# Optimization experiments

Measured on AMD Instinct MI355X. Metric: run time of the kernel, lower is better.

Reference implementation:

```python
import jax, jax.numpy as jnp
import numpy as np

B, D, CL, QL = 32, 128, 1024, 512


def setup_inputs() -> dict:
    key = jax.random.key(0)
    kC, kQ, kW = jax.random.split(key, 3)
    C = jax.random.normal(kC, (B, D, CL), dtype=jnp.float32)
    Q = jax.random.normal(kQ, (B, D, QL), dtype=jnp.float32)
    # xavier_normal_ on (B*CL, 1, 3D): std = sqrt(2 / (fan_in + fan_out)) = sqrt(2/(1+3D))
    std = (2.0 / (1.0 + 3.0 * D)) ** 0.5
    W = jax.random.normal(kW, (B * CL, 1, 3 * D), dtype=jnp.float32) * std
    return {"C": C, "Q": Q, "W": W}


def reference(C, Q, W):
    # C: (B, D, CL), Q: (B, D, QL), W: (B*CL, 1, 3D)
    b, d, cl = C.shape
    Ct = jnp.transpose(C, (0, 2, 1))   # (B, CL, D)
    Qt = jnp.transpose(Q, (0, 2, 1))   # (B, QL, D)
    Wr = W.reshape(b, cl, 3 * d)
    wq, wc, wqc = Wr[..., :d], Wr[..., d:2 * d], Wr[..., 2 * d:]
    # Trilinear similarity: S[b,c,q] = wq[b,c].Q[b,q] + wc[b,c].C[b,c] + wqc[b,c].(C[b,c]*Q[b,q])
    S = (jnp.einsum('bcd,bqd->bcq', wq, Qt)
         + jnp.sum(wc * Ct, axis=-1, keepdims=True)
         + jnp.einsum('bcd,bqd->bcq', wqc * Ct, Qt))   # (B, CL, QL)
    S1 = jax.nn.softmax(S, axis=2)  # over queries
    S2 = jax.nn.softmax(S, axis=1)  # over context
    A = jnp.einsum('bcq,bqd->bcd', S1, Qt)             # (B, CL, D)
    # B = (S1 @ S2^T) @ C, reassociated as S1 @ (S2^T @ C) to avoid (CL,CL) intermediate
    S2tC = jnp.einsum('bkq,bkd->bqd', S2, Ct)          # (B, QL, D)
    Bm = jnp.einsum('bcq,bqd->bcd', S1, S2tC)          # (B, CL, D)
    out = jnp.concatenate([Ct, A, Ct * A, Ct * Bm], axis=2)  # (B, CL, 4D)
    # dropout is identity in eval mode
    return jnp.transpose(out, (0, 2, 1))               # (B, 4D, CL)
```

## Files before the change

### kernel.cpp

```cpp
#include <hip/hip_runtime.h>
#include <hip/hip_bf16.h>
#include <cstddef>

#define B_  32
#define D_  128
#define CL_ 1024
#define QL_ 512

using short8  = __attribute__((ext_vector_type(8))) short;
using short4v = __attribute__((ext_vector_type(4))) short;
using float4v = __attribute__((ext_vector_type(4))) float;

__device__ __forceinline__ unsigned short f2bf(float f) {
    unsigned int u = __float_as_uint(f);
    u += 0x7FFFu + ((u >> 16) & 1u);
    return (unsigned short)(u >> 16);
}
__device__ __forceinline__ float bf2f(unsigned short h) {
    return __uint_as_float(((unsigned int)h) << 16);
}

__device__ __forceinline__ void swz_bt(int i, int& b, int& t) {
    b = (i & 7) + 8 * (i >> 7);
    t = (i >> 3) & 15;
}

__global__ __launch_bounds__(256) void k_u_bias(const float* __restrict__ C,
                                                const float* __restrict__ W,
                                                unsigned short* __restrict__ U,
                                                float* __restrict__ bias,
                                                unsigned short* __restrict__ Cbf) {
    int b  = blockIdx.y;
    int c0 = blockIdx.x * 32;
    int tid = threadIdx.x;

    __shared__ float tile[128][33];
    __shared__ float bred[32][9];

    for (int pass = 0; pass < 16; ++pass) {
        int d = pass * 8 + (tid >> 5);
        int c = tid & 31;
        float v = C[((size_t)(b * D_ + d)) * CL_ + c0 + c];
        tile[d][c] = v;
        Cbf[((size_t)(b * D_ + d)) * CL_ + c0 + c] = f2bf(v);
    }
    __syncthreads();

    int tc    = tid >> 3;
    int lane8 = tid & 7;
    int c     = c0 + tc;
    size_t wbase = ((size_t)(b * CL_ + c)) * (3 * D_);
    size_t ubase = ((size_t)(b * CL_ + c)) * D_;

    float bpart = 0.f;
    #pragma unroll
    for (int i = 0; i < 4; ++i) {
        int d = i * 32 + lane8 * 4;
        float4 wq4  = *(const float4*)(W + wbase + d);
        float4 wc4  = *(const float4*)(W + wbase + D_ + d);
        float4 wqc4 = *(const float4*)(W + wbase + 2 * D_ + d);
        float ct0 = tile[d + 0][tc], ct1 = tile[d + 1][tc];
        float ct2 = tile[d + 2][tc], ct3 = tile[d + 3][tc];
        short4v u;
        u[0] = (short)f2bf(wq4.x + wqc4.x * ct0);
        u[1] = (short)f2bf(wq4.y + wqc4.y * ct1);
        u[2] = (short)f2bf(wq4.z + wqc4.z * ct2);
        u[3] = (short)f2bf(wq4.w + wqc4.w * ct3);
        *(short4v*)(U + ubase + d) = u;
        bpart += wc4.x * ct0 + wc4.y * ct1 + wc4.z * ct2 + wc4.w * ct3;
    }
    bred[tc][lane8] = bpart;
    __syncthreads();
    if (lane8 == 0) {
        float s = 0.f;
        for (int i = 0; i < 8; ++i) s += bred[tc][i];
        bias[b * CL_ + c] = s;
    }
}

__global__ __launch_bounds__(256) void k_qt(const float* __restrict__ Q,
                                            unsigned short* __restrict__ Qt,
                                            unsigned short* __restrict__ Qbf) {
    int b  = blockIdx.z;
    int d0 = blockIdx.y * 64;
    int q0 = blockIdx.x * 64;
    int tid = threadIdx.x;
    __shared__ float t[64][65];
    for (int p = 0; p < 16; ++p) {
        int d = p * 4 + (tid >> 6);
        int q = tid & 63;
        float v = Q[((size_t)(b * D_ + d0 + d)) * QL_ + q0 + q];
        t[d][q] = v;
        Qbf[((size_t)(b * D_ + d0 + d)) * QL_ + q0 + q] = f2bf(v);
    }
    __syncthreads();
    for (int p = 0; p < 16; ++p) {
        int q  = p * 4 + (tid >> 6);
        int dd = tid & 63;
        Qt[((size_t)(b * QL_ + q0 + q)) * D_ + d0 + dd] = f2bf(t[dd][q]);
    }
}

__global__ __launch_bounds__(256) void k_gs2(const unsigned short* __restrict__ Ubf,
                                             const unsigned short* __restrict__ Qtbf,
                                             const float* __restrict__ bias,
                                             unsigned short* __restrict__ Sbf,
                                             float* __restrict__ rmax,
                                             float* __restrict__ rinv,
                                             float* __restrict__ pcmax,
                                             float* __restrict__ pcsum) {
    int b, mt;
    swz_bt(blockIdx.x, b, mt);
    int m0 = mt * 64;
    int tid  = threadIdx.x;
    int lane = tid & 63, wave = tid >> 6;
    int wm = wave >> 1, wn = wave & 1;
    int quad = lane >> 4, l15 = lane & 15;

    __shared__ __align__(16) short As[64][136];
    __shared__ __align__(16) short Bs[2][64][136];
    __shared__ float sbias[64];
    __shared__ float rmw[2][64], rsw[2][64];
    __shared__ float cmw[2][8][64], csw[2][8][64];

    const unsigned short* Ab = Ubf  + ((size_t)(b * CL_ + m0)) * D_;
    const unsigned short* Bb = Qtbf + ((size_t)(b * QL_)) * D_;

    #pragma unroll
    for (int i = 0; i < 4; ++i) {
        int flat = tid + i * 256;
        int row = flat >> 4, col = (flat & 15) * 8;
        *(short8*)&As[row][col]    = *(const short8*)(Ab + (size_t)row * D_ + col);
        *(short8*)&Bs[0][row][col] = *(const short8*)(Bb + (size_t)row * D_ + col);
    }
    if (tid < 64) sbias[tid] = bias[b * CL_ + m0 + tid];

    float rm_run[2][4], rs_run[2][4];
    #pragma unroll
    for (int fi = 0; fi < 2; ++fi)
        #pragma unroll
        for (int rr = 0; rr < 4; ++rr) { rm_run[fi][rr] = -1e30f; rs_run[fi][rr] = 0.f; }

    short8 pre[4];
    for (int chunk = 0; chunk < 8; ++chunk) {
        int cur = chunk & 1;
        if (chunk < 7) {
            #pragma unroll
            for (int i = 0; i < 4; ++i) {
                int flat = tid + i * 256;
                int row = flat >> 4, col = (flat & 15) * 8;
                pre[i] = *(const short8*)(Bb + (size_t)((chunk + 1) * 64 + row) * D_ + col);
            }
        }
        __syncthreads();

        float4v acc[2][2] = {};
        #pragma unroll
        for (int ks = 0; ks < 128; ks += 32) {
            short8 af0 = *(const short8*)&As[wm * 32 + l15][ks + quad * 8];
            short8 af1 = *(const short8*)&As[wm * 32 + 16 + l15][ks + quad * 8];
            short8 bf0 = *(const short8*)&Bs[cur][wn * 32 + l15][ks + quad * 8];
            short8 bf1 = *(const short8*)&Bs[cur][wn * 32 + 16 + l15][ks + quad * 8];
            acc[0][0] = __builtin_amdgcn_mfma_f32_16x16x32_bf16(af0, bf0, acc[0][0], 0, 0, 0);
            acc[0][1] = __builtin_amdgcn_mfma_f32_16x16x32_bf16(af0, bf1, acc[0][1], 0, 0, 0);
            acc[1][0] = __builtin_amdgcn_mfma_f32_16x16x32_bf16(af1, bf0, acc[1][0], 0, 0, 0);
            acc[1][1] = __builtin_amdgcn_mfma_f32_16x16x32_bf16(af1, bf1, acc[1][1], 0, 0, 0);
        }

        float v[2][2][4];
        #pragma unroll
        for (int fi = 0; fi < 2; ++fi)
            #pragma unroll
            for (int fj = 0; fj < 2; ++fj)
                #pragma unroll
                for (int rr = 0; rr < 4; ++rr) {
                    int mloc = wm * 32 + fi * 16 + quad * 4 + rr;
                    float x = acc[fi][fj][rr] + sbias[mloc];
                    v[fi][fj][rr] = x;
                    int nloc = wn * 32 + fj * 16 + l15;
                    Sbf[((size_t)(b * CL_ + m0 + mloc)) * QL_ + chunk * 64 + nloc] = f2bf(x);
                }

        #pragma unroll
        for (int fi = 0; fi < 2; ++fi)
            #pragma unroll
            for (int rr = 0; rr < 4; ++rr) {
                float v0 = v[fi][0][rr], v1 = v[fi][1][rr];
                float nm = fmaxf(rm_run[fi][rr], fmaxf(v0, v1));
                rs_run[fi][rr] = rs_run[fi][rr] * __expf(rm_run[fi][rr] - nm)
                               + __expf(v0 - nm) + __expf(v1 - nm);
                rm_run[fi][rr] = nm;
            }

        #pragma unroll
        for (int fj = 0; fj < 2; ++fj) {
            float cm = v[0][fj][0];
            #pragma unroll
            for (int fi = 0; fi < 2; ++fi)
                #pragma unroll
                for (int rr = 0; rr < 4; ++rr) cm = fmaxf(cm, v[fi][fj][rr]);
            float cs = 0.f;
            #pragma unroll
            for (int fi = 0; fi < 2; ++fi)
                #pragma unroll
                for (int rr = 0; rr < 4; ++rr) cs += __expf(v[fi][fj][rr] - cm);
            #pragma unroll
            for (int off = 16; off <= 32; off <<= 1) {
                float om = __shfl_xor(cm, off);
                float os = __shfl_xor(cs, off);
                float nm = fmaxf(cm, om);
                cs = cs * __expf(cm - nm) + os * __expf(om - nm);
                cm = nm;
            }
            if (quad == 0) {
                int col = wn * 32 + fj * 16 + l15;
                cmw[wm][chunk][col] = cm;
                csw[wm][chunk][col] = cs;
            }
        }

        if (chunk < 7) {
            #pragma unroll
            for (int i = 0; i < 4; ++i) {
                int flat = tid + i * 256;
                int row = flat >> 4, col = (flat & 15) * 8;
                *(short8*)&Bs[cur ^ 1][row][col] = pre[i];
            }
        }
    }
    __syncthreads();

    #pragma unroll
    for (int e = 0; e < 2; ++e) {
        int idx = tid + e * 256;
        int ch = idx >> 6, col = idx & 63;
        float m0v = cmw[0][ch][col], m1v = cmw[1][ch][col];
        float nm = fmaxf(m0v, m1v);
        float ss = csw[0][ch][col] * __expf(m0v - nm) + csw[1][ch][col] * __expf(m1v - nm);
        size_t pi = ((size_t)(b * 16 + mt)) * QL_ + ch * 64 + col;
        pcmax[pi] = nm;
        pcsum[pi] = ss;
    }

    #pragma unroll
    for (int off = 1; off <= 8; off <<= 1)
        #pragma unroll
        for (int fi = 0; fi < 2; ++fi)
            #pragma unroll
            for (int rr = 0; rr < 4; ++rr) {
                float om = __shfl_xor(rm_run[fi][rr], off);
                float os = __shfl_xor(rs_run[fi][rr], off);
                float nm = fmaxf(rm_run[fi][rr], om);
                rs_run[fi][rr] = rs_run[fi][rr] * __expf(rm_run[fi][rr] - nm)
                               + os * __expf(om - nm);
                rm_run[fi][rr] = nm;
            }
    if (l15 == 0) {
        #pragma unroll
        for (int fi = 0; fi < 2; ++fi)
            #pragma unroll
            for (int rr = 0; rr < 4; ++rr) {
                int m = wm * 32 + fi * 16 + quad * 4 + rr;
                rmw[wn][m] = rm_run[fi][rr];
                rsw[wn][m] = rs_run[fi][rr];
            }
    }
    __syncthreads();
    if (tid < 64) {
        float m0v = rmw[0][tid], s0v = rsw[0][tid];
        float m1v = rmw[1][tid], s1v = rsw[1][tid];
        float nm = fmaxf(m0v, m1v);
        float ss = s0v * __expf(m0v - nm) + s1v * __expf(m1v - nm);
        rmax[b * CL_ + m0 + tid] = nm;
        rinv[b * CL_ + m0 + tid] = 1.0f / ss;
    }
}

__global__ __launch_bounds__(256) void k_gp(const unsigned short* __restrict__ Cbf,
                                            const unsigned short* __restrict__ Sbf,
                                            const float* __restrict__ pcmax,
                                            const float* __restrict__ pcsum,
                                            unsigned short* __restrict__ Pbf) {
    int b, qt;
    swz_bt(blockIdx.x, b, qt);
    int q0 = qt * 32;

    int tid  = threadIdx.x;
    int lane = tid & 63, wave = tid >> 6;
    int quad = lane >> 4, l15 = lane & 15;

    __shared__ __align__(16) short As[2][128][72];
    __shared__ __align__(16) short Bs[2][32][72];
    __shared__ float scm[32], sci[32];

    const unsigned short* Cb = Cbf + (size_t)b * D_ * CL_;
    const unsigned short* Sb = Sbf + (size_t)b * CL_ * QL_;

    int arow = tid >> 3;
    int acol = (tid & 7) * 8;
    int srow = tid >> 4;
    int uq   = tid & 15;

    short8 apre[4];
    unsigned int spre[4];

    #pragma unroll
    for (int p = 0; p < 4; ++p)
        apre[p] = *(const short8*)(Cb + (size_t)(p * 32 + arow) * CL_ + acol);
    #pragma unroll
    for (int p = 0; p < 4; ++p)
        spre[p] = *(const unsigned int*)(Sb + (size_t)(p * 16 + srow) * QL_ + q0 + 2 * uq);

    if (tid < 32) {
        float M = -1e30f, SS = 0.f;
        #pragma unroll
        for (int ch = 0; ch < 16; ++ch) {
            size_t idx = ((size_t)(b * 16 + ch)) * QL_ + q0 + tid;
            float m = pcmax[idx], s = pcsum[idx];
            float nM = fmaxf(M, m);
            SS = SS * __expf(M - nM) + s * __expf(m - nM);
            M = nM;
        }
        scm[tid] = M;
        sci[tid] = 1.0f / SS;
    }
    __syncthreads();

    #pragma unroll
    for (int p = 0; p < 4; ++p)
        *(short8*)&As[0][p * 32 + arow][acol] = apre[p];
    #pragma unroll
    for (int p = 0; p < 4; ++p) {
        int crow = p * 16 + srow;
        unsigned int raw = spre[p];
        float v0 = __expf(bf2f((unsigned short)(raw & 0xFFFF)) - scm[2 * uq]) * sci[2 * uq];
        float v1 = __expf(bf2f((unsigned short)(raw >> 16)) - scm[2 * uq + 1]) * sci[2 * uq + 1];
        Bs[0][2 * uq][crow]     = (short)f2bf(v0);
        Bs[0][2 * uq + 1][crow] = (short)f2bf(v1);
    }

    float4v acc[2][2] = {};

    for (int step = 0; step < 16; ++step) {
        int cur = step & 1;
        int k0n = (step + 1) * 64;
        if (step < 15) {
            #pragma unroll
            for (int p = 0; p < 4; ++p)
                apre[p] = *(const short8*)(Cb + (size_t)(p * 32 + arow) * CL_ + k0n + acol);
            #pragma unroll
            for (int p = 0; p < 4; ++p)
                spre[p] = *(const unsigned int*)(Sb + (size_t)(k0n + p * 16 + srow) * QL_ + q0 + 2 * uq);
        }
        __syncthreads();

        #pragma unroll
        for (int ks = 0; ks < 64; ks += 32) {
            short8 a0 = *(const short8*)&As[cur][wave * 32 + l15][ks + quad * 8];
            short8 a1 = *(const short8*)&As[cur][wave * 32 + 16 + l15][ks + quad * 8];
            short8 b0 = *(const short8*)&Bs[cur][l15][ks + quad * 8];
            short8 b1 = *(const short8*)&Bs[cur][16 + l15][ks + quad * 8];
            acc[0][0] = __builtin_amdgcn_mfma_f32_16x16x32_bf16(a0, b0, acc[0][0], 0, 0, 0);
            acc[0][1] = __builtin_amdgcn_mfma_f32_16x16x32_bf16(a0, b1, acc[0][1], 0, 0, 0);
            acc[1][0] = __builtin_amdgcn_mfma_f32_16x16x32_bf16(a1, b0, acc[1][0], 0, 0, 0);
            acc[1][1] = __builtin_amdgcn_mfma_f32_16x16x32_bf16(a1, b1, acc[1][1], 0, 0, 0);
        }

        if (step < 15) {
            #pragma unroll
            for (int p = 0; p < 4; ++p)
                *(short8*)&As[cur ^ 1][p * 32 + arow][acol] = apre[p];
            #pragma unroll
            for (int p = 0; p < 4; ++p) {
                int crow = p * 16 + srow;
                unsigned int raw = spre[p];
                float v0 = __expf(bf2f((unsigned short)(raw & 0xFFFF)) - scm[2 * uq]) * sci[2 * uq];
                float v1 = __expf(bf2f((unsigned short)(raw >> 16)) - scm[2 * uq + 1]) * sci[2 * uq + 1];
                Bs[cur ^ 1][2 * uq][crow]     = (short)f2bf(v0);
                Bs[cur ^ 1][2 * uq + 1][crow] = (short)f2bf(v1);
            }
        }
    }

    #pragma unroll
    for (int fi = 0; fi < 2; ++fi)
        #pragma unroll
        for (int fj = 0; fj < 2; ++fj)
            #pragma unroll
            for (int rr = 0; rr < 4; ++rr) {
                int d = wave * 32 + fi * 16 + quad * 4 + rr;
                int q = q0 + fj * 16 + l15;
                Pbf[((size_t)(b * D_ + d)) * QL_ + q] = f2bf(acc[fi][fj][rr]);
            }
}

__global__ __launch_bounds__(256) void k_av2(const unsigned short* __restrict__ Qbf,
                                             const unsigned short* __restrict__ Pbf,
                                             const unsigned short* __restrict__ Sbf,
                                             const float* __restrict__ rmax,
                                             const float* __restrict__ rinv,
                                             const float* __restrict__ C,
                                             float* __restrict__ out) {
    int b, nt;
    swz_bt(blockIdx.x, b, nt);
    int n0 = nt * 64;

    int tid  = threadIdx.x;
    int lane = tid & 63, wave = tid >> 6;
    int wm = wave >> 1, wn = wave & 1;
    int quad = lane >> 4, l15 = lane & 15;

    __shared__ __align__(16) short AsQ[128][72];
    __shared__ __align__(16) short AsP[128][72];
    __shared__ __align__(16) short Bs[64][72];
    __shared__ float srm[64], sri[64];

    if (tid < 64) {
        srm[tid] = rmax[b * CL_ + n0 + tid];
        sri[tid] = rinv[b * CL_ + n0 + tid];
    }

    const unsigned short* Qb = Qbf + (size_t)b * D_ * QL_;
    const unsigned short* Pb = Pbf + (size_t)b * D_ * QL_;
    const unsigned short* Sb = Sbf + ((size_t)(b * CL_ + n0)) * QL_;

    int arow = tid >> 3;
    int acol = (tid & 7) * 8;
    int brow = tid >> 2;
    int bcol = (tid & 3) * 16;

    short8 qa[4], pa[4];
    uint4 sraw[2];
    #pragma unroll
    for (int p = 0; p < 4; ++p) {
        int row = p * 32 + arow;
        qa[p] = *(const short8*)(Qb + (size_t)row * QL_ + acol);
        pa[p] = *(const short8*)(Pb + (size_t)row * QL_ + acol);
    }
    #pragma unroll
    for (int h = 0; h < 2; ++h)
        sraw[h] = *(const uint4*)(Sb + (size_t)brow * QL_ + bcol + h * 8);

    __syncthreads();
    float brm = srm[brow], bri = sri[brow];

    float4v accQ[4][2] = {};
    float4v accP[4][2] = {};

    for (int k0 = 0; k0 < QL_; k0 += 64) {
        #pragma unroll
        for (int p = 0; p < 4; ++p) {
            int row = p * 32 + arow;
            *(short8*)&AsQ[row][acol] = qa[p];
            *(short8*)&AsP[row][acol] = pa[p];
        }
        #pragma unroll
        for (int h = 0; h < 2; ++h) {
            unsigned int rw[4] = {sraw[h].x, sraw[h].y, sraw[h].z, sraw[h].w};
            short8 vv;
            #pragma unroll
            for (int j = 0; j < 8; ++j) {
                unsigned short bits = (unsigned short)((rw[j >> 1] >> ((j & 1) * 16)) & 0xFFFF);
                vv[j] = (short)f2bf(__expf(bf2f(bits) - brm) * bri);
            }
            *(short8*)&Bs[brow][bcol + h * 8] = vv;
        }
        __syncthreads();

        if (k0 + 64 < QL_) {
            #pragma unroll
            for (int p = 0; p < 4; ++p) {
                int row = p * 32 + arow;
                qa[p] = *(const short8*)(Qb + (size_t)row * QL_ + k0 + 64 + acol);
                pa[p] = *(const short8*)(Pb + (size_t)row * QL_ + k0 + 64 + acol);
            }
            #pragma unroll
            for (int h = 0; h < 2; ++h)
                sraw[h] = *(const uint4*)(Sb + (size_t)brow * QL_ + k0 + 64 + bcol + h * 8);
        }

        #pragma unroll
        for (int ks = 0; ks < 64; ks += 32) {
            short8 b0 = *(const short8*)&Bs[wn * 32 + l15][ks + quad * 8];
            short8 b1 = *(const short8*)&Bs[wn * 32 + 16 + l15][ks + quad * 8];
            #pragma unroll
            for (int fi = 0; fi < 4; ++fi) {
                short8 aq = *(const short8*)&AsQ[wm * 64 + fi * 16 + l15][ks + quad * 8];
                accQ[fi][0] = __builtin_amdgcn_mfma_f32_16x16x32_bf16(aq, b0, accQ[fi][0], 0, 0, 0);
                accQ[fi][1] = __builtin_amdgcn_mfma_f32_16x16x32_bf16(aq, b1, accQ[fi][1], 0, 0, 0);
            }
            #pragma unroll
            for (int fi = 0; fi < 4; ++fi) {
                short8 ap = *(const short8*)&AsP[wm * 64 + fi * 16 + l15][ks + quad * 8];
                accP[fi][0] = __builtin_amdgcn_mfma_f32_16x16x32_bf16(ap, b0, accP[fi][0], 0, 0, 0);
                accP[fi][1] = __builtin_amdgcn_mfma_f32_16x16x32_bf16(ap, b1, accP[fi][1], 0, 0, 0);
            }
        }
        __syncthreads();
    }

    #pragma unroll
    for (int fi = 0; fi < 4; ++fi)
        #pragma unroll
        for (int fj = 0; fj < 2; ++fj)
            #pragma unroll
            for (int rr = 0; rr < 4; ++rr) {
                int d = wm * 64 + fi * 16 + quad * 4 + rr;
                int c = n0 + wn * 32 + fj * 16 + l15;
                float ct = C[((size_t)(b * D_ + d)) * CL_ + c];
                float vq = accQ[fi][fj][rr];
                float vp = accP[fi][fj][rr];
                size_t ob = ((size_t)(b * 4 * D_ + d)) * CL_ + c;
                out[ob]                        = ct;
                out[ob + (size_t)D_ * CL_]     = vq;
                out[ob + 2 * (size_t)D_ * CL_] = ct * vq;
                out[ob + 3 * (size_t)D_ * CL_] = ct * vp;
            }
}

extern "C" void kernel_launch(void* const* d_in, const int* in_sizes, int n_in,
                              void* d_out, int out_size, void* d_ws, size_t ws_size,
                              hipStream_t stream) {
    const float* C = (const float*)d_in[0];
    const float* Q = (const float*)d_in[1];
    const float* W = (const float*)d_in[2];
    float* out = (float*)d_out;

    unsigned short* Ubf  = (unsigned short*)d_ws;
    unsigned short* Qtbf = Ubf  + (size_t)B_ * CL_ * D_;
    unsigned short* Qbf  = Qtbf + (size_t)B_ * QL_ * D_;
    unsigned short* Cbf  = Qbf  + (size_t)B_ * D_ * QL_;
    unsigned short* Pbf  = Cbf  + (size_t)B_ * D_ * CL_;
    unsigned short* Sbf  = Pbf  + (size_t)B_ * D_ * QL_;
    float* bias  = (float*)(Sbf + (size_t)B_ * CL_ * QL_);
    float* rmax  = bias  + (size_t)B_ * CL_;
    float* rinv  = rmax  + (size_t)B_ * CL_;
    float* pcmax = rinv  + (size_t)B_ * CL_;
    float* pcsum = pcmax + (size_t)B_ * 16 * QL_;

    k_u_bias<<<dim3(CL_ / 32, B_), 256, 0, stream>>>(C, W, Ubf, bias, Cbf);
    k_qt<<<dim3(QL_ / 64, D_ / 64, B_), 256, 0, stream>>>(Q, Qtbf, Qbf);
    k_gs2<<<512, 256, 0, stream>>>(Ubf, Qtbf, bias, Sbf, rmax, rinv, pcmax, pcsum);
    k_gp<<<512, 256, 0, stream>>>(Cbf, Sbf, pcmax, pcsum, Pbf);
    k_av2<<<512, 256, 0, stream>>>(Qbf, Pbf, Sbf, rmax, rinv, C, out);
}
```

Measured before the change: 188.9 us.

## Merge preprocessing kernels and halve tiles in gp/av2 for more blocks

Fuses the U/bias and Q-transpose preprocessing kernels into one launch that branches on block index. Splits k_gp along D into two halves and shrinks k_av2's context tile from 64 to 32, doubling both grids to 1024 blocks to improve occupancy and wave-level parallelism. k_av2 now reads Q and P A-operands straight from global memory instead of staging them in LDS, and double-buffers the softmax B tile. The trade-off is more redundant S reads and exp work across blocks, plus uncached global operand loads in the inner loop.

```diff
diff --git a/kernel.cpp b/kernel.cpp
--- a/kernel.cpp
+++ b/kernel.cpp
@@ -24,80 +24,87 @@
     b = (i & 7) + 8 * (i >> 7);
     t = (i >> 3) & 15;
 }
-
-__global__ __launch_bounds__(256) void k_u_bias(const float* __restrict__ C,
-                                                const float* __restrict__ W,
-                                                unsigned short* __restrict__ U,
-                                                float* __restrict__ bias,
-                                                unsigned short* __restrict__ Cbf) {
-    int b  = blockIdx.y;
-    int c0 = blockIdx.x * 32;
+__device__ __forceinline__ void swz32(int i, int& b, int& t) {
+    b = (i & 7) + 8 * (i >> 8);
+    t = (i >> 3) & 31;
+}
+
+__global__ __launch_bounds__(256) void k_pre(const float* __restrict__ C,
+                                             const float* __restrict__ W,
+                                             unsigned short* __restrict__ U,
+                                             float* __restrict__ bias,
+                                             unsigned short* __restrict__ Cbf,
+                                             const float* __restrict__ Q,
+                                             unsigned short* __restrict__ Qt,
+                                             unsigned short* __restrict__ Qbf) {
+    __shared__ __align__(16) float smf[4608];
     int tid = threadIdx.x;
 
-    __shared__ float tile[128][33];
-    __shared__ float bred[32][9];
-
-    for (int pass = 0; pass < 16; ++pass) {
-        int d = pass * 8 + (tid >> 5);
-        int c = tid & 31;
-        float v = C[((size_t)(b * D_ + d)) * CL_ + c0 + c];
-        tile[d][c] = v;
-        Cbf[((size_t)(b * D_ + d)) * CL_ + c0 + c] = f2bf(v);
-    }
-    __syncthreads();
-
-    int tc    = tid >> 3;
-    int lane8 = tid & 7;
-    int c     = c0 + tc;
-    size_t wbase = ((size_t)(b * CL_ + c)) * (3 * D_);
-    size_t ubase = ((size_t)(b * CL_ + c)) * D_;
-
-    float bpart = 0.f;
-    #pragma unroll
-    for (int i = 0; i < 4; ++i) {
-        int d = i * 32 + lane8 * 4;
-        float4 wq4  = *(const float4*)(W + wbase + d);
-        float4 wc4  = *(const float4*)(W + wbase + D_ + d);
-        float4 wqc4 = *(const float4*)(W + wbase + 2 * D_ + d);
-        float ct0 = tile[d + 0][tc], ct1 = tile[d + 1][tc];
-        float ct2 = tile[d + 2][tc], ct3 = tile[d + 3][tc];
-        short4v u;
-        u[0] = (short)f2bf(wq4.x + wqc4.x * ct0);
-        u[1] = (short)f2bf(wq4.y + wqc4.y * ct1);
-        u[2] = (short)f2bf(wq4.z + wqc4.z * ct2);
-        u[3] = (short)f2bf(wq4.w + wqc4.w * ct3);
-        *(short4v*)(U + ubase + d) = u;
-        bpart += wc4.x * ct0 + wc4.y * ct1 + wc4.z * ct2 + wc4.w * ct3;
-    }
-    bred[tc][lane8] = bpart;
-    __syncthreads();
-    if (lane8 == 0) {
-        float s = 0.f;
-        for (int i = 0; i < 8; ++i) s += bred[tc][i];
-        bias[b * CL_ + c] = s;
-    }
-}
-
-__global__ __launch_bounds__(256) void k_qt(const float* __restrict__ Q,
-                                            unsigned short* __restrict__ Qt,
-                                            unsigned short* __restrict__ Qbf) {
-    int b  = blockIdx.z;
-    int d0 = blockIdx.y * 64;
-    int q0 = blockIdx.x * 64;
-    int tid = threadIdx.x;
-    __shared__ float t[64][65];
-    for (int p = 0; p < 16; ++p) {
-        int d = p * 4 + (tid >> 6);
-        int q = tid & 63;
-        float v = Q[((size_t)(b * D_ + d0 + d)) * QL_ + q0 + q];
-        t[d][q] = v;
-        Qbf[((size_t)(b * D_ + d0 + d)) * QL_ + q0 + q] = f2bf(v);
-    }
-    __syncthreads();
-    for (int p = 0; p < 16; ++p) {
-        int q  = p * 4 + (tid >> 6);
-        int dd = tid & 63;
-        Qt[((size_t)(b * QL_ + q0 + q)) * D_ + d0 + dd] = f2bf(t[dd][q]);
+    if (blockIdx.x < 1024) {
+        int b  = blockIdx.x >> 5;
+        int c0 = (blockIdx.x & 31) * 32;
+        float (*tile)[33] = (float(*)[33])smf;
+        float (*bred)[9]  = (float(*)[9])(smf + 4224);
+
+        for (int pass = 0; pass < 16; ++pass) {
+            int d = pass * 8 + (tid >> 5);
+            int c = tid & 31;
+            float v = C[((size_t)(b * D_ + d)) * CL_ + c0 + c];
+            tile[d][c] = v;
+            Cbf[((size_t)(b * D_ + d)) * CL_ + c0 + c] = f2bf(v);
+        }
+        __syncthreads();
+
+        int tc    = tid >> 3;
+        int lane8 = tid & 7;
+        int c     = c0 + tc;
+        size_t wbase = ((size_t)(b * CL_ + c)) * (3 * D_);
+        size_t ubase = ((size_t)(b * CL_ + c)) * D_;
+
+        float bpart = 0.f;
+        #pragma unroll
+        for (int i = 0; i < 4; ++i) {
+            int d = i * 32 + lane8 * 4;
+            float4 wq4  = *(const float4*)(W + wbase + d);
+            float4 wc4  = *(const float4*)(W + wbase + D_ + d);
+            float4 wqc4 = *(const float4*)(W + wbase + 2 * D_ + d);
+            float ct0 = tile[d + 0][tc], ct1 = tile[d + 1][tc];
+            float ct2 = tile[d + 2][tc], ct3 = tile[d + 3][tc];
+            short4v u;
+            u[0] = (short)f2bf(wq4.x + wqc4.x * ct0);
+            u[1] = (short)f2bf(wq4.y + wqc4.y * ct1);
+            u[2] = (short)f2bf(wq4.z + wqc4.z * ct2);
+            u[3] = (short)f2bf(wq4.w + wqc4.w * ct3);
+            *(short4v*)(U + ubase + d) = u;
+            bpart += wc4.x * ct0 + wc4.y * ct1 + wc4.z * ct2 + wc4.w * ct3;
+        }
+        bred[tc][lane8] = bpart;
+        __syncthreads();
+        if (lane8 == 0) {
+            float s = 0.f;
+            for (int i = 0; i < 8; ++i) s += bred[tc][i];
+            bias[b * CL_ + c] = s;
+        }
+    } else {
+        int j  = blockIdx.x - 1024;
+        int b  = j >> 4;
+        int d0 = ((j >> 3) & 1) * 64;
+        int q0 = (j & 7) * 64;
+        float (*t)[65] = (float(*)[65])smf;
+
+        for (int p = 0; p < 16; ++p) {
+            int d = p * 4 + (tid >> 6);
+            int q = tid & 63;
+            float v = Q[((size_t)(b * D_ + d0 + d)) * QL_ + q0 + q];
+            t[d][q] = v;
+            Qbf[((size_t)(b * D_ + d0 + d)) * QL_ + q0 + q] = f2bf(v);
+        }
+        __syncthreads();
+        for (int p = 0; p < 16; ++p) {
+            int q  = p * 4 + (tid >> 6);
+            int dd = tid & 63;
+            Qt[((size_t)(b * QL_ + q0 + q)) * D_ + d0 + dd] = f2bf(t[dd][q]);
+        }
     }
 }
 
@@ -281,32 +288,33 @@
                                             const float* __restrict__ pcmax,
                                             const float* __restrict__ pcsum,
                                             unsigned short* __restrict__ Pbf) {
-    int b, qt;
-    swz_bt(blockIdx.x, b, qt);
-    int q0 = qt * 32;
+    int b, t;
+    swz32(blockIdx.x, b, t);
+    int qt = t & 15, dh = t >> 4;
+    int q0 = qt * 32, d0 = dh * 64;
 
     int tid  = threadIdx.x;
     int lane = tid & 63, wave = tid >> 6;
     int quad = lane >> 4, l15 = lane & 15;
 
-    __shared__ __align__(16) short As[2][128][72];
+    __shared__ __align__(16) short As[2][64][72];
     __shared__ __align__(16) short Bs[2][32][72];
     __shared__ float scm[32], sci[32];
 
-    const unsigned short* Cb = Cbf + (size_t)b * D_ * CL_;
+    const unsigned short* Cb = Cbf + ((size_t)(b * D_ + d0)) * CL_;
     const unsigned short* Sb = Sbf + (size_t)b * CL_ * QL_;
 
-    int arow = tid >> 3;
-    int acol = (tid & 7) * 8;
+    int arow = tid >> 2;
+    int acol = (tid & 3) * 16;
     int srow = tid >> 4;
     int uq   = tid & 15;
 
-    short8 apre[4];
+    short8 apre[2];
     unsigned int spre[4];
 
     #pragma unroll
-    for (int p = 0; p < 4; ++p)
-        apre[p] = *(const short8*)(Cb + (size_t)(p * 32 + arow) * CL_ + acol);
+    for (int p = 0; p < 2; ++p)
+        apre[p] = *(const short8*)(Cb + (size_t)arow * CL_ + acol + p * 8);
     #pragma unroll
     for (int p = 0; p < 4; ++p)
         spre[p] = *(const unsigned int*)(Sb + (size_t)(p * 16 + srow) * QL_ + q0 + 2 * uq);
@@ -327,8 +335,8 @@
     __syncthreads();
 
     #pragma unroll
-    for (int p = 0; p < 4; ++p)
-        *(short8*)&As[0][p * 32 + arow][acol] = apre[p];
+    for (int p = 0; p < 2; ++p)
+        *(short8*)&As[0][arow][acol + p * 8] = apre[p];
     #pragma unroll
     for (int p = 0; p < 4; ++p) {
         int crow = p * 16 + srow;
@@ -339,15 +347,15 @@
         Bs[0][2 * uq + 1][crow] = (short)f2bf(v1);
     }
 
-    float4v acc[2][2] = {};
+    float4v acc[2] = {};
 
     for (int step = 0; step < 16; ++step) {
         int cur = step & 1;
         int k0n = (step + 1) * 64;
         if (step < 15) {
             #pragma unroll
-            for (int p = 0; p < 4; ++p)
-                apre[p] = *(const short8*)(Cb + (size_t)(p * 32 + arow) * CL_ + k0n + acol);
+            for (int p = 0; p < 2; ++p)
+                apre[p] = *(const short8*)(Cb + (size_t)arow * CL_ + k0n + acol + p * 8);
             #pragma unroll
             for (int p = 0; p < 4; ++p)
                 spre[p] = *(const unsigned int*)(Sb + (size_t)(k0n + p * 16 + srow) * QL_ + q0 + 2 * uq);
@@ -356,20 +364,17 @@
 
         #pragma unroll
         for (int ks = 0; ks < 64; ks += 32) {
-            short8 a0 = *(const short8*)&As[cur][wave * 32 + l15][ks + quad * 8];
-            short8 a1 = *(const short8*)&As[cur][wave * 32 + 16 + l15][ks + quad * 8];
+            short8 a  = *(const short8*)&As[cur][wave * 16 + l15][ks + quad * 8];
             short8 b0 = *(const short8*)&Bs[cur][l15][ks + quad * 8];
             short8 b1 = *(const short8*)&Bs[cur][16 + l15][ks + quad * 8];
-            acc[0][0] = __builtin_amdgcn_mfma_f32_16x16x32_bf16(a0, b0, acc[0][0], 0, 0, 0);
-            acc[0][1] = __builtin_amdgcn_mfma_f32_16x16x32_bf16(a0, b1, acc[0][1], 0, 0, 0);
-            acc[1][0] = __builtin_amdgcn_mfma_f32_16x16x32_bf16(a1, b0, acc[1][0], 0, 0, 0);
-            acc[1][1] = __builtin_amdgcn_mfma_f32_16x16x32_bf16(a1, b1, acc[1][1], 0, 0, 0);
+            acc[0] = __builtin_amdgcn_mfma_f32_16x16x32_bf16(a, b0, acc[0], 0, 0, 0);
+            acc[1] = __builtin_amdgcn_mfma_f32_16x16x32_bf16(a, b1, acc[1], 0, 0, 0);
         }
 
         if (step < 15) {
             #pragma unroll
-            for (int p = 0; p < 4; ++p)
-                *(short8*)&As[cur ^ 1][p * 32 + arow][acol] = apre[p];
+            for (int p = 0; p < 2; ++p)
+                *(short8*)&As[cur ^ 1][arow][acol + p * 8] = apre[p];
             #pragma unroll
             for (int p = 0; p < 4; ++p) {
                 int crow = p * 16 + srow;
@@ -383,15 +388,13 @@
     }
 
     #pragma unroll
-    for (int fi = 0; fi < 2; ++fi)
-        #pragma unroll
-        for (int fj = 0; fj < 2; ++fj)
-            #pragma unroll
-            for (int rr = 0; rr < 4; ++rr) {
-                int d = wave * 32 + fi * 16 + quad * 4 + rr;
-                int q = q0 + fj * 16 + l15;
-                Pbf[((size_t)(b * D_ + d)) * QL_ + q] = f2bf(acc[fi][fj][rr]);
-            }
+    for (int fj = 0; fj < 2; ++fj)
+        #pragma unroll
+        for (int rr = 0; rr < 4; ++rr) {
+            int d = d0 + wave * 16 + quad * 4 + rr;
+            int q = q0 + fj * 16 + l15;
+            Pbf[((size_t)(b * D_ + d)) * QL_ + q] = f2bf(acc[fj][rr]);
+        }
 }
 
 __global__ __launch_bounds__(256) void k_av2(const unsigned short* __restrict__ Qbf,
@@ -402,20 +405,17 @@
                                              const float* __restrict__ C,
                                              float* __restrict__ out) {
     int b, nt;
-    swz_bt(blockIdx.x, b, nt);
-    int n0 = nt * 64;
+    swz32(blockIdx.x, b, nt);
+    int n0 = nt * 32;
 
     int tid  = threadIdx.x;
     int lane = tid & 63, wave = tid >> 6;
-    int wm = wave >> 1, wn = wave & 1;
     int quad = lane >> 4, l15 = lane & 15;
 
-    __shared__ __align__(16) short AsQ[128][72];
-    __shared__ __align__(16) short AsP[128][72];
-    __shared__ __align__(16) short Bs[64][72];
-    __shared__ float srm[64], sri[64];
-
-    if (tid < 64) {
+    __shared__ __align__(16) short Bs[2][32][72];
+    __shared__ float srm[32], sri[32];
+
+    if (tid < 32) {
         srm[tid] = rmax[b * CL_ + n0 + tid];
         sri[tid] = rinv[b * CL_ + n0 + tid];
     }
@@ -424,89 +424,74 @@
     const unsigned short* Pb = Pbf + (size_t)b * D_ * QL_;
     const unsigned short* Sb = Sbf + ((size_t)(b * CL_ + n0)) * QL_;
 
-    int arow = tid >> 3;
-    int acol = (tid & 7) * 8;
-    int brow = tid >> 2;
-    int bcol = (tid & 3) * 16;
-
-    short8 qa[4], pa[4];
-    uint4 sraw[2];
-    #pragma unroll
-    for (int p = 0; p < 4; ++p) {
-        int row = p * 32 + arow;
-        qa[p] = *(const short8*)(Qb + (size_t)row * QL_ + acol);
-        pa[p] = *(const short8*)(Pb + (size_t)row * QL_ + acol);
-    }
-    #pragma unroll
-    for (int h = 0; h < 2; ++h)
-        sraw[h] = *(const uint4*)(Sb + (size_t)brow * QL_ + bcol + h * 8);
-
+    int brow = tid >> 3;
+    int bcol = (tid & 7) * 8;
+
+    uint4 sraw = *(const uint4*)(Sb + (size_t)brow * QL_ + bcol);
     __syncthreads();
     float brm = srm[brow], bri = sri[brow];
 
-    float4v accQ[4][2] = {};
-    float4v accP[4][2] = {};
-
-    for (int k0 = 0; k0 < QL_; k0 += 64) {
-        #pragma unroll
-        for (int p = 0; p < 4; ++p) {
-            int row = p * 32 + arow;
-            *(short8*)&AsQ[row][acol] = qa[p];
-            *(short8*)&AsP[row][acol] = pa[p];
-        }
-        #pragma unroll
-        for (int h = 0; h < 2; ++h) {
-            unsigned int rw[4] = {sraw[h].x, sraw[h].y, sraw[h].z, sraw[h].w};
+    {
+        unsigned int rw[4] = {sraw.x, sraw.y, sraw.z, sraw.w};
+        short8 vv;
+        #pragma unroll
+        for (int j = 0; j < 8; ++j) {
+            unsigned short bits = (unsigned short)((rw[j >> 1] >> ((j & 1) * 16)) & 0xFFFF);
+            vv[j] = (short)f2bf(__expf(bf2f(bits) - brm) * bri);
+        }
+        *(short8*)&Bs[0][brow][bcol] = vv;
+    }
+
+    float4v accQ[2][2] = {};
+    float4v accP[2][2] = {};
+
+    for (int step = 0; step < 8; ++step) {
+        int cur = step & 1;
+        int k0 = step * 64;
+        if (step < 7)
+            sraw = *(const uint4*)(Sb + (size_t)brow * QL_ + k0 + 64 + bcol);
+        __syncthreads();
+
+        #pragma unroll
+        for (int ks = 0; ks < 64; ks += 32) {
+            short8 b0 = *(const short8*)&Bs[cur][l15][ks + quad * 8];
+            short8 b1 = *(const short8*)&Bs[cur][16 + l15][ks + quad * 8];
+            #pragma unroll
+            for (int fi = 0; fi < 2; ++fi) {
+                int row = wave * 32 + fi * 16 + l15;
+                short8 aq = *(const short8*)(Qb + (size_t)row * QL_ + k0 + ks + quad * 8);
+                accQ[fi][0] = __builtin_amdgcn_mfma_f32_16x16x32_bf16(aq, b0, accQ[fi][0], 0, 0, 0);
+                accQ[fi][1] = __builtin_amdgcn_mfma_f32_16x16x32_bf16(aq, b1, accQ[fi][1], 0, 0, 0);
+            }
+            #pragma unroll
+            for (int fi = 0; fi < 2; ++fi) {
+                int row = wave * 32 + fi * 16 + l15;
+                short8 ap = *(const short8*)(Pb + (size_t)row * QL_ + k0 + ks + quad * 8);
+                accP[fi][0] = __builtin_amdgcn_mfma_f32_16x16x32_bf16(ap, b0, accP[fi][0], 0, 0, 0);
+                accP[fi][1] = __builtin_amdgcn_mfma_f32_16x16x32_bf16(ap, b1, accP[fi][1], 0, 0, 0);
+            }
+        }
+
+        if (step < 7) {
+            unsigned int rw[4] = {sraw.x, sraw.y, sraw.z, sraw.w};
             short8 vv;
             #pragma unroll
             for (int j = 0; j < 8; ++j) {
                 unsigned short bits = (unsigned short)((rw[j >> 1] >> ((j & 1) * 16)) & 0xFFFF);
                 vv[j] = (short)f2bf(__expf(bf2f(bits) - brm) * bri);
             }
-            *(short8*)&Bs[brow][bcol + h * 8] = vv;
-        }
-        __syncthreads();
-
-        if (k0 + 64 < QL_) {
-            #pragma unroll
-            for (int p = 0; p < 4; ++p) {
-                int row = p * 32 + arow;
-                qa[p] = *(const short8*)(Qb + (size_t)row * QL_ + k0 + 64 + acol);
-                pa[p] = *(const short8*)(Pb + (size_t)row * QL_ + k0 + 64 + acol);
-            }
-            #pragma unroll
-            for (int h = 0; h < 2; ++h)
-                sraw[h] = *(const uint4*)(Sb + (size_t)brow * QL_ + k0 + 64 + bcol + h * 8);
-        }
-
-        #pragma unroll
-        for (int ks = 0; ks < 64; ks += 32) {
-            short8 b0 = *(const short8*)&Bs[wn * 32 + l15][ks + quad * 8];
-            short8 b1 = *(const short8*)&Bs[wn * 32 + 16 + l15][ks + quad * 8];
-            #pragma unroll
-            for (int fi = 0; fi < 4; ++fi) {
-                short8 aq = *(const short8*)&AsQ[wm * 64 + fi * 16 + l15][ks + quad * 8];
-                accQ[fi][0] = __builtin_amdgcn_mfma_f32_16x16x32_bf16(aq, b0, accQ[fi][0], 0, 0, 0);
-                accQ[fi][1] = __builtin_amdgcn_mfma_f32_16x16x32_bf16(aq, b1, accQ[fi][1], 0, 0, 0);
-            }
-            #pragma unroll
-            for (int fi = 0; fi < 4; ++fi) {
-                short8 ap = *(const short8*)&AsP[wm * 64 + fi * 16 + l15][ks + quad * 8];
-                accP[fi][0] = __builtin_amdgcn_mfma_f32_16x16x32_bf16(ap, b0, accP[fi][0], 0, 0, 0);
-                accP[fi][1] = __builtin_amdgcn_mfma_f32_16x16x32_bf16(ap, b1, accP[fi][1], 0, 0, 0);
-            }
-        }
-        __syncthreads();
-    }
-
-    #pragma unroll
-    for (int fi = 0; fi < 4; ++fi)
+            *(short8*)&Bs[cur ^ 1][brow][bcol] = vv;
+        }
+    }
+
+    #pragma unroll
+    for (int fi = 0; fi < 2; ++fi)
         #pragma unroll
         for (int fj = 0; fj < 2; ++fj)
             #pragma unroll
             for (int rr = 0; rr < 4; ++rr) {
-                int d = wm * 64 + fi * 16 + quad * 4 + rr;
-                int c = n0 + wn * 32 + fj * 16 + l15;
+                int d = wave * 32 + fi * 16 + quad * 4 + rr;
+                int c = n0 + fj * 16 + l15;
                 float ct = C[((size_t)(b * D_ + d)) * CL_ + c];
                 float vq = accQ[fi][fj][rr];
                 float vp = accP[fi][fj][rr];
@@ -538,9 +523,8 @@
     float* pcmax = rinv  + (size_t)B_ * CL_;
     float* pcsum = pcmax + (size_t)B_ * 16 * QL_;
 
-    k_u_bias<<<dim3(CL_ / 32, B_), 256, 0, stream>>>(C, W, Ubf, bias, Cbf);
-    k_qt<<<dim3(QL_ / 64, D_ / 64, B_), 256, 0, stream>>>(Q, Qtbf, Qbf);
+    k_pre<<<1536, 256, 0, stream>>>(C, W, Ubf, bias, Cbf, Q, Qtbf, Qbf);
     k_gs2<<<512, 256, 0, stream>>>(Ubf, Qtbf, bias, Sbf, rmax, rinv, pcmax, pcsum);
-    k_gp<<<512, 256, 0, stream>>>(Cbf, Sbf, pcmax, pcsum, Pbf);
-    k_av2<<<512, 256, 0, stream>>>(Qbf, Pbf, Sbf, rmax, rinv, C, out);
-}
+    k_gp<<<1024, 256, 0, stream>>>(Cbf, Sbf, pcmax, pcsum, Pbf);
+    k_av2<<<1024, 256, 0, stream>>>(Qbf, Pbf, Sbf, rmax, rinv, C, out);
+}
```

After: 202.1 us. 1.07x slower.
